# Performance work log

Measured on AMD Instinct MI355X. Metric: run time of the kernel, lower is better.

## Reference

```python
import jax, jax.numpy as jnp
import numpy as np

B, N, F_IN, F, C, E = 8192, 68, 2, 128, 16, 272
EPS = 1e-15


def graph_conv(x, src, dst, W_rel, W_root, b):
    # PyG GraphConv (aggr='add'): out_i = W_rel @ sum_{j->i} x_j + W_root @ x_i + b
    agg = jnp.zeros(x.shape, x.dtype).at[:, dst].add(x[:, src])  # [B,N,Fin]
    return agg @ W_rel.T + x @ W_root.T + b


def setup_inputs() -> dict:
    key = jax.random.key(0)
    ks = jax.random.split(key, 12)
    x = jax.random.normal(ks[0], (B, N, F_IN), jnp.float32)
    edge_index = jax.random.randint(ks[1], (2, E), 0, N, jnp.int32)
    adj = jax.random.uniform(ks[2], (B, N, N), jnp.float32)
    s = jax.random.normal(ks[3], (B, N, C), jnp.float32)
    pos = jax.random.normal(ks[4], (B, N, F_IN), jnp.float32)
    sc = 0.1
    W1_rel = jax.random.normal(ks[5], (F, F_IN), jnp.float32) * sc
    W1_root = jax.random.normal(ks[6], (F, F_IN), jnp.float32) * sc
    b1 = jnp.zeros((F,), jnp.float32)
    W2_rel = jax.random.normal(ks[7], (F, F), jnp.float32) * sc
    W2_root = jax.random.normal(ks[8], (F, F), jnp.float32) * sc
    b2 = jnp.zeros((F,), jnp.float32)
    W3_rel = jax.random.normal(ks[9], (F, F), jnp.float32) * sc
    W3_root = jax.random.normal(ks[10], (F, F), jnp.float32) * sc
    b3 = jnp.zeros((F,), jnp.float32)
    return dict(x=x, edge_index=edge_index, adj=adj, s=s, pos=pos,
                W1_rel=W1_rel, W1_root=W1_root, b1=b1,
                W2_rel=W2_rel, W2_root=W2_root, b2=b2,
                W3_rel=W3_rel, W3_root=W3_root, b3=b3)


def reference(x, edge_index, adj, s, pos,
              W1_rel, W1_root, b1, W2_rel, W2_root, b2, W3_rel, W3_root, b3):
    src, dst = edge_index[0], edge_index[1]
    h = jax.nn.relu(graph_conv(x, src, dst, W1_rel, W1_root, b1))
    h = jax.nn.relu(graph_conv(h, src, dst, W2_rel, W2_root, b2))
    h = jax.nn.relu(graph_conv(h, src, dst, W3_rel, W3_root, b3))  # [B,N,F]
    # dense_diff_pool
    s_sm = jax.nn.softmax(s, axis=-1)                       # [B,N,C]
    out = jnp.einsum('bnc,bnf->bcf', s_sm, h)               # [B,C,F]
    out_adj = jnp.einsum('bnc,bnm,bmk->bck', s_sm, adj, s_sm)  # [B,C,C]
    diff = adj - jnp.einsum('bnc,bmc->bnm', s_sm, s_sm)
    link_loss = jnp.sqrt(jnp.sum(diff * diff)) / adj.size
    ent_loss = jnp.mean(jnp.sum(-s_sm * jnp.log(s_sm + EPS), axis=-1))
    return (out, out_adj, link_loss, ent_loss, pos)
```

## Files before the change

### kernel.cpp

```cpp
#include <hip/hip_runtime.h>
#include <math.h>

#define B_   8192
#define N_   68
#define FIN  2
#define F_   128
#define C_   16
#define E_   272

#define OUT_OFF  0
#define ADJ_OFF  (B_*C_*F_)
#define LINK_IDX (ADJ_OFF + B_*C_*C_)
#define ENT_IDX  (LINK_IDX + 1)
#define POS_OFF  (ENT_IDX + 1)

#define WS_CSR_OFF  131072
#define WS_W_OFF    133120
#define WS_AG_OFF   264192

typedef __attribute__((ext_vector_type(8))) short bf16x8;
typedef __attribute__((ext_vector_type(4))) float f32x4;

#define SWZ256(r, cb) (((r) * 256) + ((cb) ^ (((r) & 7) << 4)))
#define SWZ512(r, cb) (((r) * 512) + ((cb) ^ (((r) & 7) << 4)))
#define SWZH(r, cb)   (((r) * 192) + ((cb) ^ (((r) & 3) << 4)))
#define MFMA16(a, bb, c) __builtin_amdgcn_mfma_f32_16x16x32_bf16((a), (bb), (c), 0, 0, 0)

__device__ __forceinline__ short bf16_rne(float x) {
  unsigned u = __builtin_bit_cast(unsigned, x);
  u += 0x7FFFu + ((u >> 16) & 1u);
  return (short)(u >> 16);
}
__device__ __forceinline__ short4 pack4(f32x4 v) {
  short4 s;
  s.x = bf16_rne(v[0]); s.y = bf16_rne(v[1]); s.z = bf16_rne(v[2]); s.w = bf16_rne(v[3]);
  return s;
}

__global__ void prep_kernel(const int* __restrict__ edge_index,
                            const float* __restrict__ W2r, const float* __restrict__ W2o,
                            const float* __restrict__ W3r, const float* __restrict__ W3o,
                            int* __restrict__ csr, short* __restrict__ wcat,
                            short* __restrict__ agw) {
  int gid = blockIdx.x * blockDim.x + threadIdx.x;
  for (int e = gid; e < 2 * F_ * 256; e += gridDim.x * blockDim.x) {
    int layer = e >> 15, idx = e & 32767;
    int j = idx >> 8, k = idx & 255;
    const float* Wr = layer ? W3r : W2r;
    const float* Wo = layer ? W3o : W2o;
    float v = (k < F_) ? Wr[j * F_ + k] : Wo[j * F_ + (k - F_)];
    wcat[e] = bf16_rne(v);
  }
  __shared__ unsigned short cnt[80 * 128];
  __shared__ int src_s[E_], dst_s[E_], cc[N_], offs[N_ + 1];
  if (blockIdx.x == 0) {
    int t = threadIdx.x;
    for (int i = t; i < 80 * 128; i += blockDim.x) cnt[i] = 0;
    for (int e = t; e < E_; e += blockDim.x) { src_s[e] = edge_index[e]; dst_s[e] = edge_index[E_ + e]; }
    for (int n = t; n < N_; n += blockDim.x) cc[n] = 0;
    __syncthreads();
    if (t == 0) {
      for (int e = 0; e < E_; ++e) { cnt[dst_s[e] * 128 + src_s[e]]++; cc[dst_s[e]]++; }
      offs[0] = 0;
      for (int n = 0; n < N_; ++n) offs[n + 1] = offs[n] + cc[n];
      for (int n = 0; n < N_; ++n) cc[n] = offs[n];
      for (int e = 0; e < E_; ++e) { int d = dst_s[e]; csr[N_ + 1 + cc[d]++] = src_s[e]; }
      for (int n = 0; n <= N_; ++n) csr[n] = offs[n];
    }
    __syncthreads();
    for (int i = t; i < 80 * 128; i += blockDim.x) agw[i] = bf16_rne((float)cnt[i]);
  }
}

__device__ __forceinline__ void layer_mfma(short* Hn, short* UT,
    const short* __restrict__ wl, const float* __restrict__ bias,
    const short* __restrict__ agw,
    int hinB, int houtB, int outT, int l15, int lg, int j0)
{
  bf16x8 Ar[4], Ao[4];
#pragma unroll
  for (int ks = 0; ks < 4; ++ks) {
    Ar[ks] = *(const bf16x8*)(wl + (j0 + l15) * 256 + ks * 32 + 8 * lg);
    Ao[ks] = *(const bf16x8*)(wl + (j0 + l15) * 256 + 128 + ks * 32 + 8 * lg);
  }
  f32x4 U0 = {0,0,0,0}, U1 = {0,0,0,0}, U2 = {0,0,0,0}, U3 = {0,0,0,0}, U4 = {0,0,0,0};
  f32x4 V0 = {0,0,0,0}, V1 = {0,0,0,0}, V2 = {0,0,0,0}, V3 = {0,0,0,0}, V4 = {0,0,0,0};
#define G1_(UN, VN, NT) do { \
  _Pragma("unroll") \
  for (int ks = 0; ks < 4; ++ks) { \
    bf16x8 b_ = *(const bf16x8*)((const char*)Hn + SWZ512((NT) * 16 + l15, hinB + ks * 64 + 16 * lg)); \
    UN = MFMA16(Ar[ks], b_, UN); \
    VN = MFMA16(Ao[ks], b_, VN); \
  } \
} while (0)
  G1_(U0, V0, 0); G1_(U1, V1, 1); G1_(U2, V2, 2); G1_(U3, V3, 3); G1_(U4, V4, 4);
#undef G1_
#define UTW_(UN, NT) do { \
  _Pragma("unroll") \
  for (int q = 0; q < 4; ++q) \
    *(short*)((char*)UT + SWZH(j0 + lg * 4 + q, ((NT) * 16 + l15) * 2)) = bf16_rne(UN[q]); \
} while (0)
  UTW_(U0, 0); UTW_(U1, 1); UTW_(U2, 2); UTW_(U3, 3); UTW_(U4, 4);
#undef UTW_
  bf16x8 aU[3];
#pragma unroll
  for (int ks = 0; ks < 3; ++ks)
    aU[ks] = *(const bf16x8*)((const char*)UT + SWZH(j0 + l15, ks * 64 + 16 * lg));
  float4 bv = *(const float4*)&bias[j0 + lg * 4];
#define G2_(VN, NT) do { \
  f32x4 acc = {0.f, 0.f, 0.f, 0.f}; \
  _Pragma("unroll") \
  for (int ks = 0; ks < 3; ++ks) \
    acc = MFMA16(aU[ks], *(const bf16x8*)(agw + ((NT) * 16 + l15) * 128 + ks * 32 + lg * 8), acc); \
  f32x4 v_; \
  v_[0] = fmaxf(acc[0] + VN[0] + bv.x, 0.f); \
  v_[1] = fmaxf(acc[1] + VN[1] + bv.y, 0.f); \
  v_[2] = fmaxf(acc[2] + VN[2] + bv.z, 0.f); \
  v_[3] = fmaxf(acc[3] + VN[3] + bv.w, 0.f); \
  if (!outT) { \
    *(short4*)((char*)Hn + SWZ512((NT) * 16 + l15, houtB + (j0 + lg * 4) * 2)) = pack4(v_); \
  } else { \
    _Pragma("unroll") \
    for (int q = 0; q < 4; ++q) \
      *(short*)((char*)UT + SWZH(j0 + lg * 4 + q, ((NT) * 16 + l15) * 2)) = bf16_rne(v_[q]); \
  } \
} while (0)
  G2_(V0, 0); G2_(V1, 1); G2_(V2, 2); G2_(V3, 3); G2_(V4, 4);
#undef G2_
}

__launch_bounds__(512, 4)
__global__ void layers_kernel(
    const float* __restrict__ x, const float* __restrict__ s,
    const float* __restrict__ W1r, const float* __restrict__ W1o, const float* __restrict__ b1,
    const float* __restrict__ b2f, const float* __restrict__ b3f,
    const short* __restrict__ wcat, const short* __restrict__ agw,
    float* __restrict__ out, const int* __restrict__ csr)
{
  __shared__ __align__(16) short Hn[80 * 256];
  __shared__ __align__(16) short UT[128 * 96];
  __shared__ __align__(16) short ssmT[16 * 128];
  __shared__ float xb[N_ * FIN], axb[N_ * FIN];
  __shared__ int offs[N_ + 1], srcs[E_];

  const int b = blockIdx.x, tid = threadIdx.x;
  const int lane = tid & 63, wave = tid >> 6;
  const int l15 = lane & 15, lg = lane >> 4;
  const int j0 = wave * 16;

  for (int i = tid; i < N_ + 1; i += 512) offs[i] = csr[i];
  for (int i = tid; i < E_; i += 512) srcs[i] = csr[N_ + 1 + i];
  for (int i = tid; i < N_ * FIN; i += 512) xb[i] = x[(size_t)b * N_ * FIN + i];
  {
    int4 zz; zz.x = 0; zz.y = 0; zz.z = 0; zz.w = 0;
    for (int i = tid; i < 384; i += 512) {
      int r = 68 + (i >> 5), cb = (i & 31) * 16;
      *(int4*)((char*)Hn + SWZ512(r, cb)) = zz;
    }
    long long z8 = 0;
    for (int i = tid; i < 128 * 2; i += 512) {
      int r = i >> 1, cb = 160 + (i & 1) * 16;
      *(int4*)((char*)UT + SWZH(r, cb)) = zz;
    }
    for (int i = tid; i < 16 * 7; i += 512) {
      int r = i / 7, cb = 136 + (i % 7) * 8;
      *(long long*)((char*)ssmT + SWZ256(r, cb)) = z8;
    }
  }
  if (tid < N_) {
    const float* srow = &s[((size_t)b * N_ + tid) * C_];
    float sv[16];
    float mx = -1e30f;
#pragma unroll
    for (int c = 0; c < 16; ++c) { sv[c] = srow[c]; mx = fmaxf(mx, sv[c]); }
    float sum = 0.f;
#pragma unroll
    for (int c = 0; c < 16; ++c) { sv[c] = expf(sv[c] - mx); sum += sv[c]; }
    float inv = 1.f / sum;
#pragma unroll
    for (int c = 0; c < 16; ++c)
      *(short*)((char*)ssmT + SWZ256(c, tid * 2)) = bf16_rne(sv[c] * inv);
  }
  __syncthreads();

  if (tid < N_) {
    float a0 = 0, a1 = 0;
    for (int e = offs[tid]; e < offs[tid + 1]; ++e) {
      int sr = srcs[e];
      a0 += xb[sr * 2]; a1 += xb[sr * 2 + 1];
    }
    axb[tid * 2] = a0; axb[tid * 2 + 1] = a1;
  }
  __syncthreads();

  {
    int f4 = (tid & 31) * 4;
    float4 R0 = *(const float4*)&W1r[f4 * 2], R1 = *(const float4*)&W1r[f4 * 2 + 4];
    float4 O0 = *(const float4*)&W1o[f4 * 2], O1 = *(const float4*)&W1o[f4 * 2 + 4];
    float4 Bv = *(const float4*)&b1[f4];
#pragma unroll
    for (int p = 0; p < 5; ++p) {
      int n = p * 16 + (tid >> 5);
      if (n < N_) {
        float a0 = axb[n * 2], a1 = axb[n * 2 + 1], x0 = xb[n * 2], x1 = xb[n * 2 + 1];
        f32x4 v;
        v[0] = fmaxf(a0 * R0.x + a1 * R0.y + x0 * O0.x + x1 * O0.y + Bv.x, 0.f);
        v[1] = fmaxf(a0 * R0.z + a1 * R0.w + x0 * O0.z + x1 * O0.w + Bv.y, 0.f);
        v[2] = fmaxf(a0 * R1.x + a1 * R1.y + x0 * O1.x + x1 * O1.y + Bv.z, 0.f);
        v[3] = fmaxf(a0 * R1.z + a1 * R1.w + x0 * O1.z + x1 * O1.w + Bv.w, 0.f);
        *(short4*)((char*)Hn + SWZ512(n, f4 * 2)) = pack4(v);
      }
    }
  }
  __syncthreads();

  layer_mfma(Hn, UT, wcat, b2f, agw, 0, 256, 0, l15, lg, j0);
  __syncthreads();

  layer_mfma(Hn, UT, wcat + 32768, b3f, agw, 256, 0, 1, l15, lg, j0);

  {
    f32x4 acc = {0.f, 0.f, 0.f, 0.f};
#pragma unroll
    for (int ks = 0; ks < 3; ++ks)
      acc = MFMA16(*(const bf16x8*)((const char*)UT + SWZH(j0 + l15, ks * 64 + 16 * lg)),
                   *(const bf16x8*)((const char*)ssmT + SWZ256(l15, ks * 64 + 16 * lg)), acc);
    float4 st; st.x = acc[0]; st.y = acc[1]; st.z = acc[2]; st.w = acc[3];
    *(float4*)&out[OUT_OFF + (size_t)b * C_ * F_ + l15 * F_ + j0 + lg * 4] = st;
  }
}

__launch_bounds__(512, 4)
__global__ void pool_kernel(
    const float* __restrict__ adj, const float* __restrict__ s, const float* __restrict__ pos,
    float* __restrict__ out, double* __restrict__ partials)
{
  __shared__ __align__(16) short AdjB[80 * 128];
  __shared__ __align__(16) short ssmT[16 * 128];
  __shared__ __align__(16) short TT[16 * 128];
  __shared__ double red[16];

  const int b = blockIdx.x, tid = threadIdx.x;
  const int lane = tid & 63, wave = tid >> 6;
  const int l15 = lane & 15, lg = lane >> 4;

  {
    long long z8 = 0;
    for (int i = tid; i < 1200; i += 512) {
      int r = i / 15, cb = 136 + (i % 15) * 8;
      *(long long*)((char*)AdjB + SWZ256(r, cb)) = z8;
    }
    for (int i = tid; i < 204; i += 512) {
      int r = 68 + i / 17, cb = (i % 17) * 8;
      *(long long*)((char*)AdjB + SWZ256(r, cb)) = z8;
    }
    for (int i = tid; i < 16 * 7; i += 512) {
      int r = i / 7, cb = 136 + (i % 7) * 8;
      *(long long*)((char*)ssmT + SWZ256(r, cb)) = z8;
      *(long long*)((char*)TT + SWZ256(r, cb)) = z8;
    }
  }
  float sadj2 = 0.f;
  const float* adjb = &adj[(size_t)b * N_ * N_];
  for (int q = tid; q < N_ * N_; q += 512) {
    int n = q / N_, m = q - n * N_;
    float v = adjb[q];
    sadj2 += v * v;
    *(short*)((char*)AdjB + SWZ256(n, m * 2)) = bf16_rne(v);
  }
  float entPart = 0.f;
  if (tid < N_) {
    const float* srow = &s[((size_t)b * N_ + tid) * C_];
    float sv[16], ev[16];
    float mx = -1e30f;
#pragma unroll
    for (int c = 0; c < 16; ++c) { sv[c] = srow[c]; mx = fmaxf(mx, sv[c]); }
    float sum = 0.f;
#pragma unroll
    for (int c = 0; c < 16; ++c) { ev[c] = expf(sv[c] - mx); sum += ev[c]; }
    float inv = 1.f / sum, ps = 0.f;
#pragma unroll
    for (int c = 0; c < 16; ++c) {
      float pv = ev[c] * inv;
      ps += pv * sv[c];
      *(short*)((char*)ssmT + SWZ256(c, tid * 2)) = bf16_rne(pv);
    }
    entPart = (mx + logf(sum)) - ps;
  }
  for (int i = tid; i < N_ * FIN; i += 512)
    out[POS_OFF + (size_t)b * N_ * FIN + i] = pos[(size_t)b * N_ * FIN + i];
  __syncthreads();

  float g2Part = 0.f;
  if (wave < 5) {
    f32x4 acc = {0.f, 0.f, 0.f, 0.f};
#pragma unroll
    for (int ks = 0; ks < 3; ++ks)
      acc = MFMA16(*(const bf16x8*)((const char*)AdjB + SWZ256(wave * 16 + l15, ks * 64 + 16 * lg)),
                   *(const bf16x8*)((const char*)ssmT + SWZ256(l15, ks * 64 + 16 * lg)), acc);
#pragma unroll
    for (int r = 0; r < 4; ++r) {
      int n = wave * 16 + lg * 4 + r;
      if (n < N_) *(short*)((char*)TT + SWZ256(l15, n * 2)) = bf16_rne(acc[r]);
    }
  } else if (wave == 5) {
    f32x4 acc = {0.f, 0.f, 0.f, 0.f};
#pragma unroll
    for (int ks = 0; ks < 3; ++ks) {
      bf16x8 a = *(const bf16x8*)((const char*)ssmT + SWZ256(l15, ks * 64 + 16 * lg));
      acc = MFMA16(a, a, acc);
    }
#pragma unroll
    for (int r = 0; r < 4; ++r) g2Part += acc[r] * acc[r];
  }
  __syncthreads();

  float trPart = 0.f;
  if (wave == 0) {
    f32x4 acc = {0.f, 0.f, 0.f, 0.f};
#pragma unroll
    for (int ks = 0; ks < 3; ++ks)
      acc = MFMA16(*(const bf16x8*)((const char*)ssmT + SWZ256(l15, ks * 64 + 16 * lg)),
                   *(const bf16x8*)((const char*)TT + SWZ256(l15, ks * 64 + 16 * lg)), acc);
#pragma unroll
    for (int r = 0; r < 4; ++r) {
      int c = lg * 4 + r;
      out[ADJ_OFF + (size_t)b * 256 + c * 16 + l15] = acc[r];
      if (c == l15) trPart += acc[r];
    }
  }

  double lk = (double)sadj2 - 2.0 * (double)trPart + (double)g2Part;
  double en = (double)entPart;
  for (int o = 32; o > 0; o >>= 1) { lk += __shfl_down(lk, o); en += __shfl_down(en, o); }
  if ((tid & 63) == 0) { red[wave] = lk; red[8 + wave] = en; }
  __syncthreads();
  if (tid == 0) {
    double L = 0, En = 0;
    for (int w = 0; w < 8; ++w) { L += red[w]; En += red[8 + w]; }
    partials[2 * b] = L;
    partials[2 * b + 1] = En;
  }
}

__global__ void finalize_kernel(const double* __restrict__ partials, float* __restrict__ out) {
  __shared__ double red[16];
  int tid = threadIdx.x;
  double L = 0, En = 0;
  for (int i = tid; i < B_; i += 512) { L += partials[2 * i]; En += partials[2 * i + 1]; }
  for (int o = 32; o > 0; o >>= 1) { L += __shfl_down(L, o); En += __shfl_down(En, o); }
  if ((tid & 63) == 0) { red[tid >> 6] = L; red[8 + (tid >> 6)] = En; }
  __syncthreads();
  if (tid == 0) {
    double Ls = 0, Es = 0;
    for (int w = 0; w < 8; ++w) { Ls += red[w]; Es += red[8 + w]; }
    out[LINK_IDX] = (float)(sqrt(Ls) / (double)((size_t)B_ * N_ * N_));
    out[ENT_IDX] = (float)(Es / (double)((size_t)B_ * N_));
  }
}

extern "C" void kernel_launch(void* const* d_in, const int* in_sizes, int n_in,
                              void* d_out, int out_size, void* d_ws, size_t ws_size,
                              hipStream_t stream) {
  const float* x   = (const float*)d_in[0];
  const int*   ei  = (const int*)d_in[1];
  const float* adj = (const float*)d_in[2];
  const float* s   = (const float*)d_in[3];
  const float* pos = (const float*)d_in[4];
  const float* W1r = (const float*)d_in[5];
  const float* W1o = (const float*)d_in[6];
  const float* b1  = (const float*)d_in[7];
  const float* W2r = (const float*)d_in[8];
  const float* W2o = (const float*)d_in[9];
  const float* b2  = (const float*)d_in[10];
  const float* W3r = (const float*)d_in[11];
  const float* W3o = (const float*)d_in[12];
  const float* b3  = (const float*)d_in[13];

  float* out = (float*)d_out;
  double* partials = (double*)d_ws;
  int* csr = (int*)((char*)d_ws + WS_CSR_OFF);
  short* wcat = (short*)((char*)d_ws + WS_W_OFF);
  short* agw  = (short*)((char*)d_ws + WS_AG_OFF);

  prep_kernel<<<65, 512, 0, stream>>>(ei, W2r, W2o, W3r, W3o, csr, wcat, agw);
  layers_kernel<<<B_, 512, 0, stream>>>(x, s, W1r, W1o, b1, b2, b3, wcat, agw, out, csr);
  pool_kernel<<<B_, 512, 0, stream>>>(adj, s, pos, out, partials);
  finalize_kernel<<<1, 512, 0, stream>>>(partials, out);
}
```

Measured before the change: 485.1 us.

## Fuse layers and pooling kernels into one per-batch kernel with early adj prefetch

Merges the GNN layers kernel and the diff-pool kernel into a single per-graph kernel. The softmax of s is computed once and reused for both the feature pooling and the adjacency pooling, and the UT shared buffer is reused to stage bf16 adj. The adj tile is loaded into ten registers per thread at kernel start so the global loads overlap with the layer compute. This removes one launch, the duplicate softmax and s reads, and a separate pass over the grid, at the cost of higher register pressure that may reduce occupancy.

Result: slower. 506.8 us (+4.5%).

```diff
diff --git a/kernel.cpp b/kernel.cpp
--- a/kernel.cpp
+++ b/kernel.cpp
@@ -130,18 +130,21 @@
 }
 
 __launch_bounds__(512, 4)
-__global__ void layers_kernel(
-    const float* __restrict__ x, const float* __restrict__ s,
+__global__ void main_kernel(
+    const float* __restrict__ x, const float* __restrict__ adj, const float* __restrict__ s,
+    const float* __restrict__ pos,
     const float* __restrict__ W1r, const float* __restrict__ W1o, const float* __restrict__ b1,
     const float* __restrict__ b2f, const float* __restrict__ b3f,
     const short* __restrict__ wcat, const short* __restrict__ agw,
-    float* __restrict__ out, const int* __restrict__ csr)
+    float* __restrict__ out, const int* __restrict__ csr, double* __restrict__ partials)
 {
   __shared__ __align__(16) short Hn[80 * 256];
   __shared__ __align__(16) short UT[128 * 96];
   __shared__ __align__(16) short ssmT[16 * 128];
+  __shared__ __align__(16) short TT[16 * 128];
   __shared__ float xb[N_ * FIN], axb[N_ * FIN];
   __shared__ int offs[N_ + 1], srcs[E_];
+  __shared__ double red[16];
 
   const int b = blockIdx.x, tid = threadIdx.x;
   const int lane = tid & 63, wave = tid >> 6;
@@ -151,6 +154,13 @@
   for (int i = tid; i < N_ + 1; i += 512) offs[i] = csr[i];
   for (int i = tid; i < E_; i += 512) srcs[i] = csr[N_ + 1 + i];
   for (int i = tid; i < N_ * FIN; i += 512) xb[i] = x[(size_t)b * N_ * FIN + i];
+  const float* adjb = &adj[(size_t)b * N_ * N_];
+  float av0, av1, av2, av3, av4, av5, av6, av7, av8, av9;
+#define ALD_(I) { int q_ = tid + 512 * I; av##I = (q_ < N_ * N_) ? adjb[q_] : 0.f; }
+  ALD_(0) ALD_(1) ALD_(2) ALD_(3) ALD_(4) ALD_(5) ALD_(6) ALD_(7) ALD_(8) ALD_(9)
+#undef ALD_
+  float sadj2 = av0*av0 + av1*av1 + av2*av2 + av3*av3 + av4*av4
+              + av5*av5 + av6*av6 + av7*av7 + av8*av8 + av9*av9;
   {
     int4 zz; zz.x = 0; zz.y = 0; zz.z = 0; zz.w = 0;
     for (int i = tid; i < 384; i += 512) {
@@ -165,22 +175,30 @@
     for (int i = tid; i < 16 * 7; i += 512) {
       int r = i / 7, cb = 136 + (i % 7) * 8;
       *(long long*)((char*)ssmT + SWZ256(r, cb)) = z8;
-    }
-  }
+      *(long long*)((char*)TT + SWZ256(r, cb)) = z8;
+    }
+  }
+  float entPart = 0.f;
   if (tid < N_) {
     const float* srow = &s[((size_t)b * N_ + tid) * C_];
-    float sv[16];
+    float sv[16], ev[16];
     float mx = -1e30f;
 #pragma unroll
     for (int c = 0; c < 16; ++c) { sv[c] = srow[c]; mx = fmaxf(mx, sv[c]); }
     float sum = 0.f;
 #pragma unroll
-    for (int c = 0; c < 16; ++c) { sv[c] = expf(sv[c] - mx); sum += sv[c]; }
-    float inv = 1.f / sum;
-#pragma unroll
-    for (int c = 0; c < 16; ++c)
-      *(short*)((char*)ssmT + SWZ256(c, tid * 2)) = bf16_rne(sv[c] * inv);
-  }
+    for (int c = 0; c < 16; ++c) { ev[c] = expf(sv[c] - mx); sum += ev[c]; }
+    float inv = 1.f / sum, ps = 0.f;
+#pragma unroll
+    for (int c = 0; c < 16; ++c) {
+      float pv = ev[c] * inv;
+      ps += pv * sv[c];
+      *(short*)((char*)ssmT + SWZ256(c, tid * 2)) = bf16_rne(pv);
+    }
+    entPart = (mx + logf(sum)) - ps;
+  }
+  for (int i = tid; i < N_ * FIN; i += 512)
+    out[POS_OFF + (size_t)b * N_ * FIN + i] = pos[(size_t)b * N_ * FIN + i];
   __syncthreads();
 
   if (tid < N_) {
@@ -228,67 +246,24 @@
     float4 st; st.x = acc[0]; st.y = acc[1]; st.z = acc[2]; st.w = acc[3];
     *(float4*)&out[OUT_OFF + (size_t)b * C_ * F_ + l15 * F_ + j0 + lg * 4] = st;
   }
-}
-
-__launch_bounds__(512, 4)
-__global__ void pool_kernel(
-    const float* __restrict__ adj, const float* __restrict__ s, const float* __restrict__ pos,
-    float* __restrict__ out, double* __restrict__ partials)
-{
-  __shared__ __align__(16) short AdjB[80 * 128];
-  __shared__ __align__(16) short ssmT[16 * 128];
-  __shared__ __align__(16) short TT[16 * 128];
-  __shared__ double red[16];
-
-  const int b = blockIdx.x, tid = threadIdx.x;
-  const int lane = tid & 63, wave = tid >> 6;
-  const int l15 = lane & 15, lg = lane >> 4;
+  __syncthreads();
 
   {
     long long z8 = 0;
     for (int i = tid; i < 1200; i += 512) {
       int r = i / 15, cb = 136 + (i % 15) * 8;
-      *(long long*)((char*)AdjB + SWZ256(r, cb)) = z8;
+      *(long long*)((char*)UT + SWZ256(r, cb)) = z8;
     }
     for (int i = tid; i < 204; i += 512) {
       int r = 68 + i / 17, cb = (i % 17) * 8;
-      *(long long*)((char*)AdjB + SWZ256(r, cb)) = z8;
-    }
-    for (int i = tid; i < 16 * 7; i += 512) {
-      int r = i / 7, cb = 136 + (i % 7) * 8;
-      *(long long*)((char*)ssmT + SWZ256(r, cb)) = z8;
-      *(long long*)((char*)TT + SWZ256(r, cb)) = z8;
-    }
-  }
-  float sadj2 = 0.f;
-  const float* adjb = &adj[(size_t)b * N_ * N_];
-  for (int q = tid; q < N_ * N_; q += 512) {
-    int n = q / N_, m = q - n * N_;
-    float v = adjb[q];
-    sadj2 += v * v;
-    *(short*)((char*)AdjB + SWZ256(n, m * 2)) = bf16_rne(v);
-  }
-  float entPart = 0.f;
-  if (tid < N_) {
-    const float* srow = &s[((size_t)b * N_ + tid) * C_];
-    float sv[16], ev[16];
-    float mx = -1e30f;
-#pragma unroll
-    for (int c = 0; c < 16; ++c) { sv[c] = srow[c]; mx = fmaxf(mx, sv[c]); }
-    float sum = 0.f;
-#pragma unroll
-    for (int c = 0; c < 16; ++c) { ev[c] = expf(sv[c] - mx); sum += ev[c]; }
-    float inv = 1.f / sum, ps = 0.f;
-#pragma unroll
-    for (int c = 0; c < 16; ++c) {
-      float pv = ev[c] * inv;
-      ps += pv * sv[c];
-      *(short*)((char*)ssmT + SWZ256(c, tid * 2)) = bf16_rne(pv);
-    }
-    entPart = (mx + logf(sum)) - ps;
-  }
-  for (int i = tid; i < N_ * FIN; i += 512)
-    out[POS_OFF + (size_t)b * N_ * FIN + i] = pos[(size_t)b * N_ * FIN + i];
+      *(long long*)((char*)UT + SWZ256(r, cb)) = z8;
+    }
+#define AST_(I) { int q_ = tid + 512 * I; if (q_ < N_ * N_) { \
+    int n_ = q_ / N_, m_ = q_ - n_ * N_; \
+    *(short*)((char*)UT + SWZ256(n_, m_ * 2)) = bf16_rne(av##I); } }
+    AST_(0) AST_(1) AST_(2) AST_(3) AST_(4) AST_(5) AST_(6) AST_(7) AST_(8) AST_(9)
+#undef AST_
+  }
   __syncthreads();
 
   float g2Part = 0.f;
@@ -296,7 +271,7 @@
     f32x4 acc = {0.f, 0.f, 0.f, 0.f};
 #pragma unroll
     for (int ks = 0; ks < 3; ++ks)
-      acc = MFMA16(*(const bf16x8*)((const char*)AdjB + SWZ256(wave * 16 + l15, ks * 64 + 16 * lg)),
+      acc = MFMA16(*(const bf16x8*)((const char*)UT + SWZ256(wave * 16 + l15, ks * 64 + 16 * lg)),
                    *(const bf16x8*)((const char*)ssmT + SWZ256(l15, ks * 64 + 16 * lg)), acc);
 #pragma unroll
     for (int r = 0; r < 4; ++r) {
@@ -329,7 +304,6 @@
       if (c == l15) trPart += acc[r];
     }
   }
-
   double lk = (double)sadj2 - 2.0 * (double)trPart + (double)g2Part;
   double en = (double)entPart;
   for (int o = 32; o > 0; o >>= 1) { lk += __shfl_down(lk, o); en += __shfl_down(en, o); }
@@ -384,7 +358,7 @@
   short* agw  = (short*)((char*)d_ws + WS_AG_OFF);
 
   prep_kernel<<<65, 512, 0, stream>>>(ei, W2r, W2o, W3r, W3o, csr, wcat, agw);
-  layers_kernel<<<B_, 512, 0, stream>>>(x, s, W1r, W1o, b1, b2, b3, wcat, agw, out, csr);
-  pool_kernel<<<B_, 512, 0, stream>>>(adj, s, pos, out, partials);
+  main_kernel<<<B_, 512, 0, stream>>>(x, adj, s, pos, W1r, W1o, b1, b2, b3,
+                                      wcat, agw, out, csr, partials);
   finalize_kernel<<<1, 512, 0, stream>>>(partials, out);
 }
```

## Process two graphs per pool block with vectorized float4 adjacency loads

Applied to the files above, without the earlier changes.

The pooling kernel now handles two batch elements per 512-thread block, with duplicated shared-memory buffers, interleaved MFMA chains, and B/2 blocks. Adjacency is loaded as float4 and converted four values at a time instead of scalar loads. The aim is to amortize block setup, zero-fill and sync overhead, and to raise memory-level parallelism. The cost is doubled LDS per block, which may lower occupancy. The pack4 helper is assumed to exist in the hidden code.

New measurement: 470.7 us. -3.0%, faster.

```diff
diff --git a/kernel.cpp b/kernel.cpp
--- a/kernel.cpp
+++ b/kernel.cpp
@@ -231,16 +231,17 @@
 }
 
 __launch_bounds__(512, 4)
-__global__ void pool_kernel(
+__global__ void pool2_kernel(
     const float* __restrict__ adj, const float* __restrict__ s, const float* __restrict__ pos,
     float* __restrict__ out, double* __restrict__ partials)
 {
-  __shared__ __align__(16) short AdjB[80 * 128];
-  __shared__ __align__(16) short ssmT[16 * 128];
-  __shared__ __align__(16) short TT[16 * 128];
-  __shared__ double red[16];
-
-  const int b = blockIdx.x, tid = threadIdx.x;
+  __shared__ __align__(16) short AdjA[80 * 128], AdjB2[80 * 128];
+  __shared__ __align__(16) short ssmA[16 * 128], ssmB[16 * 128];
+  __shared__ __align__(16) short TTA[16 * 128],  TTB[16 * 128];
+  __shared__ double red[32];
+
+  const int blk = blockIdx.x, tid = threadIdx.x;
+  const int gA = blk * 2, gB = blk * 2 + 1;
   const int lane = tid & 63, wave = tid >> 6;
   const int l15 = lane & 15, lg = lane >> 4;
 
@@ -248,98 +249,153 @@
     long long z8 = 0;
     for (int i = tid; i < 1200; i += 512) {
       int r = i / 15, cb = 136 + (i % 15) * 8;
-      *(long long*)((char*)AdjB + SWZ256(r, cb)) = z8;
+      *(long long*)((char*)AdjA + SWZ256(r, cb)) = z8;
+      *(long long*)((char*)AdjB2 + SWZ256(r, cb)) = z8;
     }
     for (int i = tid; i < 204; i += 512) {
       int r = 68 + i / 17, cb = (i % 17) * 8;
-      *(long long*)((char*)AdjB + SWZ256(r, cb)) = z8;
-    }
-    for (int i = tid; i < 16 * 7; i += 512) {
+      *(long long*)((char*)AdjA + SWZ256(r, cb)) = z8;
+      *(long long*)((char*)AdjB2 + SWZ256(r, cb)) = z8;
+    }
+    for (int i = tid; i < 112; i += 512) {
       int r = i / 7, cb = 136 + (i % 7) * 8;
-      *(long long*)((char*)ssmT + SWZ256(r, cb)) = z8;
-      *(long long*)((char*)TT + SWZ256(r, cb)) = z8;
-    }
-  }
-  float sadj2 = 0.f;
-  const float* adjb = &adj[(size_t)b * N_ * N_];
-  for (int q = tid; q < N_ * N_; q += 512) {
-    int n = q / N_, m = q - n * N_;
-    float v = adjb[q];
-    sadj2 += v * v;
-    *(short*)((char*)AdjB + SWZ256(n, m * 2)) = bf16_rne(v);
-  }
-  float entPart = 0.f;
-  if (tid < N_) {
-    const float* srow = &s[((size_t)b * N_ + tid) * C_];
-    float sv[16], ev[16];
-    float mx = -1e30f;
-#pragma unroll
-    for (int c = 0; c < 16; ++c) { sv[c] = srow[c]; mx = fmaxf(mx, sv[c]); }
-    float sum = 0.f;
-#pragma unroll
-    for (int c = 0; c < 16; ++c) { ev[c] = expf(sv[c] - mx); sum += ev[c]; }
-    float inv = 1.f / sum, ps = 0.f;
-#pragma unroll
-    for (int c = 0; c < 16; ++c) {
-      float pv = ev[c] * inv;
-      ps += pv * sv[c];
-      *(short*)((char*)ssmT + SWZ256(c, tid * 2)) = bf16_rne(pv);
-    }
-    entPart = (mx + logf(sum)) - ps;
-  }
-  for (int i = tid; i < N_ * FIN; i += 512)
-    out[POS_OFF + (size_t)b * N_ * FIN + i] = pos[(size_t)b * N_ * FIN + i];
-  __syncthreads();
-
-  float g2Part = 0.f;
+      *(long long*)((char*)ssmA + SWZ256(r, cb)) = z8;
+      *(long long*)((char*)ssmB + SWZ256(r, cb)) = z8;
+      *(long long*)((char*)TTA + SWZ256(r, cb)) = z8;
+      *(long long*)((char*)TTB + SWZ256(r, cb)) = z8;
+    }
+  }
+  float sadjA = 0.f, sadjB = 0.f;
+  const float* adjbA = &adj[(size_t)gA * N_ * N_];
+  const float* adjbB = &adj[(size_t)gB * N_ * N_];
+#pragma unroll
+  for (int i = 0; i < 3; ++i) {
+    int q4 = tid + 512 * i;
+    if (q4 < 1156) {
+      float4 vA = *(const float4*)&adjbA[q4 * 4];
+      float4 vB = *(const float4*)&adjbB[q4 * 4];
+      sadjA += vA.x * vA.x + vA.y * vA.y + vA.z * vA.z + vA.w * vA.w;
+      sadjB += vB.x * vB.x + vB.y * vB.y + vB.z * vB.z + vB.w * vB.w;
+      int n = q4 / 17, m4 = (q4 - n * 17) * 4;
+      f32x4 fa; fa[0] = vA.x; fa[1] = vA.y; fa[2] = vA.z; fa[3] = vA.w;
+      f32x4 fb; fb[0] = vB.x; fb[1] = vB.y; fb[2] = vB.z; fb[3] = vB.w;
+      *(short4*)((char*)AdjA + SWZ256(n, m4 * 2)) = pack4(fa);
+      *(short4*)((char*)AdjB2 + SWZ256(n, m4 * 2)) = pack4(fb);
+    }
+  }
+  float entA = 0.f, entB = 0.f;
+  {
+    bool isA = (tid < N_);
+    bool isB = (tid >= 128 && tid < 128 + N_);
+    if (isA || isB) {
+      int row = isB ? (tid - 128) : tid;
+      const float* srow = &s[((size_t)(isB ? gB : gA) * N_ + row) * C_];
+      short* ssmP = isB ? ssmB : ssmA;
+      float sv[16], ev[16];
+      float mx = -1e30f;
+#pragma unroll
+      for (int c = 0; c < 16; ++c) { sv[c] = srow[c]; mx = fmaxf(mx, sv[c]); }
+      float sum = 0.f;
+#pragma unroll
+      for (int c = 0; c < 16; ++c) { ev[c] = expf(sv[c] - mx); sum += ev[c]; }
+      float inv = 1.f / sum, ps = 0.f;
+#pragma unroll
+      for (int c = 0; c < 16; ++c) {
+        float pv = ev[c] * inv;
+        ps += pv * sv[c];
+        *(short*)((char*)ssmP + SWZ256(c, row * 2)) = bf16_rne(pv);
+      }
+      float ent = (mx + logf(sum)) - ps;
+      if (isB) entB = ent; else entA = ent;
+    }
+  }
+  for (int i = tid; i < N_ * FIN; i += 512) {
+    out[POS_OFF + (size_t)gA * N_ * FIN + i] = pos[(size_t)gA * N_ * FIN + i];
+    out[POS_OFF + (size_t)gB * N_ * FIN + i] = pos[(size_t)gB * N_ * FIN + i];
+  }
+  __syncthreads();
+
+  float g2A = 0.f, g2B = 0.f;
   if (wave < 5) {
-    f32x4 acc = {0.f, 0.f, 0.f, 0.f};
-#pragma unroll
-    for (int ks = 0; ks < 3; ++ks)
-      acc = MFMA16(*(const bf16x8*)((const char*)AdjB + SWZ256(wave * 16 + l15, ks * 64 + 16 * lg)),
-                   *(const bf16x8*)((const char*)ssmT + SWZ256(l15, ks * 64 + 16 * lg)), acc);
+    f32x4 accA = {0.f, 0.f, 0.f, 0.f};
+    f32x4 accB = {0.f, 0.f, 0.f, 0.f};
+#pragma unroll
+    for (int ks = 0; ks < 3; ++ks) {
+      accA = MFMA16(*(const bf16x8*)((const char*)AdjA + SWZ256(wave * 16 + l15, ks * 64 + 16 * lg)),
+                    *(const bf16x8*)((const char*)ssmA + SWZ256(l15, ks * 64 + 16 * lg)), accA);
+      accB = MFMA16(*(const bf16x8*)((const char*)AdjB2 + SWZ256(wave * 16 + l15, ks * 64 + 16 * lg)),
+                    *(const bf16x8*)((const char*)ssmB + SWZ256(l15, ks * 64 + 16 * lg)), accB);
+    }
 #pragma unroll
     for (int r = 0; r < 4; ++r) {
       int n = wave * 16 + lg * 4 + r;
-      if (n < N_) *(short*)((char*)TT + SWZ256(l15, n * 2)) = bf16_rne(acc[r]);
+      if (n < N_) {
+        *(short*)((char*)TTA + SWZ256(l15, n * 2)) = bf16_rne(accA[r]);
+        *(short*)((char*)TTB + SWZ256(l15, n * 2)) = bf16_rne(accB[r]);
+      }
     }
   } else if (wave == 5) {
-    f32x4 acc = {0.f, 0.f, 0.f, 0.f};
+    f32x4 accA = {0.f, 0.f, 0.f, 0.f};
+    f32x4 accB = {0.f, 0.f, 0.f, 0.f};
 #pragma unroll
     for (int ks = 0; ks < 3; ++ks) {
-      bf16x8 a = *(const bf16x8*)((const char*)ssmT + SWZ256(l15, ks * 64 + 16 * lg));
-      acc = MFMA16(a, a, acc);
-    }
-#pragma unroll
-    for (int r = 0; r < 4; ++r) g2Part += acc[r] * acc[r];
-  }
-  __syncthreads();
-
-  float trPart = 0.f;
+      bf16x8 a = *(const bf16x8*)((const char*)ssmA + SWZ256(l15, ks * 64 + 16 * lg));
+      bf16x8 b = *(const bf16x8*)((const char*)ssmB + SWZ256(l15, ks * 64 + 16 * lg));
+      accA = MFMA16(a, a, accA);
+      accB = MFMA16(b, b, accB);
+    }
+#pragma unroll
+    for (int r = 0; r < 4; ++r) { g2A += accA[r] * accA[r]; g2B += accB[r] * accB[r]; }
+  }
+  __syncthreads();
+
+  float trA = 0.f, trB = 0.f;
   if (wave == 0) {
     f32x4 acc = {0.f, 0.f, 0.f, 0.f};
 #pragma unroll
     for (int ks = 0; ks < 3; ++ks)
-      acc = MFMA16(*(const bf16x8*)((const char*)ssmT + SWZ256(l15, ks * 64 + 16 * lg)),
-                   *(const bf16x8*)((const char*)TT + SWZ256(l15, ks * 64 + 16 * lg)), acc);
+      acc = MFMA16(*(const bf16x8*)((const char*)ssmA + SWZ256(l15, ks * 64 + 16 * lg)),
+                   *(const bf16x8*)((const char*)TTA + SWZ256(l15, ks * 64 + 16 * lg)), acc);
 #pragma unroll
     for (int r = 0; r < 4; ++r) {
       int c = lg * 4 + r;
-      out[ADJ_OFF + (size_t)b * 256 + c * 16 + l15] = acc[r];
-      if (c == l15) trPart += acc[r];
-    }
-  }
-
-  double lk = (double)sadj2 - 2.0 * (double)trPart + (double)g2Part;
-  double en = (double)entPart;
-  for (int o = 32; o > 0; o >>= 1) { lk += __shfl_down(lk, o); en += __shfl_down(en, o); }
-  if ((tid & 63) == 0) { red[wave] = lk; red[8 + wave] = en; }
+      out[ADJ_OFF + (size_t)gA * 256 + c * 16 + l15] = acc[r];
+      if (c == l15) trA += acc[r];
+    }
+  } else if (wave == 1) {
+    f32x4 acc = {0.f, 0.f, 0.f, 0.f};
+#pragma unroll
+    for (int ks = 0; ks < 3; ++ks)
+      acc = MFMA16(*(const bf16x8*)((const char*)ssmB + SWZ256(l15, ks * 64 + 16 * lg)),
+                   *(const bf16x8*)((const char*)TTB + SWZ256(l15, ks * 64 + 16 * lg)), acc);
+#pragma unroll
+    for (int r = 0; r < 4; ++r) {
+      int c = lg * 4 + r;
+      out[ADJ_OFF + (size_t)gB * 256 + c * 16 + l15] = acc[r];
+      if (c == l15) trB += acc[r];
+    }
+  }
+
+  double lkA = (double)sadjA - 2.0 * (double)trA + (double)g2A;
+  double lkB = (double)sadjB - 2.0 * (double)trB + (double)g2B;
+  double enA = (double)entA, enB = (double)entB;
+  for (int o = 32; o > 0; o >>= 1) {
+    lkA += __shfl_down(lkA, o); enA += __shfl_down(enA, o);
+    lkB += __shfl_down(lkB, o); enB += __shfl_down(enB, o);
+  }
+  if ((tid & 63) == 0) {
+    red[wave] = lkA; red[8 + wave] = enA;
+    red[16 + wave] = lkB; red[24 + wave] = enB;
+  }
   __syncthreads();
   if (tid == 0) {
-    double L = 0, En = 0;
-    for (int w = 0; w < 8; ++w) { L += red[w]; En += red[8 + w]; }
-    partials[2 * b] = L;
-    partials[2 * b + 1] = En;
+    double LA = 0, EA = 0, LB = 0, EB = 0;
+    for (int w = 0; w < 8; ++w) {
+      LA += red[w]; EA += red[8 + w];
+      LB += red[16 + w]; EB += red[24 + w];
+    }
+    partials[2 * gA] = LA; partials[2 * gA + 1] = EA;
+    partials[2 * gB] = LB; partials[2 * gB + 1] = EB;
   }
 }
 
@@ -385,6 +441,6 @@
 
   prep_kernel<<<65, 512, 0, stream>>>(ei, W2r, W2o, W3r, W3o, csr, wcat, agw);
   layers_kernel<<<B_, 512, 0, stream>>>(x, s, W1r, W1o, b1, b2, b3, wcat, agw, out, csr);
-  pool_kernel<<<B_, 512, 0, stream>>>(adj, s, pos, out, partials);
+  pool2_kernel<<<B_ / 2, 512, 0, stream>>>(adj, s, pos, out, partials);
   finalize_kernel<<<1, 512, 0, stream>>>(partials, out);
 }
```
